# Performance work log

Hardware: AMD Instinct MI355X
Metric: run time of the kernel (lower is better)

Reference implementation:

```python
import jax, jax.numpy as jnp
import numpy as np

C, H, R, INTER = 1024, 16, 16, 2816  # hidden, heads, lora rank, mlp intermediate
B, N = 2, 2048
EPS = 1e-5


def setup_inputs() -> dict:
    key = jax.random.key(0)
    ks = iter(jax.random.split(key, 48))
    w = lambda shape: jax.random.normal(next(ks), shape, jnp.float32) * 0.02
    d = {}
    d["x"] = jax.random.normal(next(ks), (B, N, C), jnp.float32)
    d["y"] = jax.random.normal(next(ks), (B, N, C), jnp.float32)
    d["c"] = jax.random.normal(next(ks), (B, C), jnp.float32)
    # LayerNorms
    d["gx_w"] = jnp.ones((C,)); d["gx_b"] = jnp.zeros((C,))
    d["gy_w"] = jnp.ones((C,)); d["gy_b"] = jnp.zeros((C,))
    # adaLN: SiLU -> Linear(C, 6C)
    d["ada_w"] = w((C, 6 * C)); d["ada_b"] = jnp.zeros((6 * C,))
    # two DoRA cross-attentions
    for p in ("xy", "yx"):
        d[p + "_qkv"] = w((C, 3 * C))
        d[p + "_mag"] = jnp.ones((1, H, 1, 1))
        d[p + "_la"] = w((C, R))
        d[p + "_lb"] = w((R, C))
        d[p + "_proj"] = w((C, C))
    # two HGRN recurrent attentions
    for p in ("ax", "ay"):
        d[p + "_wi"] = w((C, C))
        d[p + "_wf"] = w((C, C))
        d[p + "_wg"] = w((C, C))
        d[p + "_wo"] = w((C, C))
        d[p + "_gn"] = jnp.ones((C,))
    # two gated MLPs
    for p in ("mx", "my"):
        d[p + "_gate"] = w((C, 2 * INTER))
        d[p + "_down"] = w((INTER, C))
    return d


def _ln(v, wgt, b):
    m = v.mean(-1, keepdims=True)
    var = ((v - m) ** 2).mean(-1, keepdims=True)
    return (v - m) / jnp.sqrt(var + EPS) * wgt + b


def _modulate(v, shift, scale):
    return v * (1.0 + scale[:, None, :]) + shift[:, None, :]


def _dora_attn(q_in, Wqkv, mag, la, lb, Wp):
    # NOTE: source ignores key/value args -> self-attention on query stream
    Bq, Nq, Cq = q_in.shape
    D = Cq // H
    qkv = (q_in @ Wqkv).reshape(Bq, Nq, 3, H, D).transpose(2, 0, 3, 1, 4)
    q, k, v = qkv[0], qkv[1], qkv[2]  # [B,H,N,D]
    delta = (q_in @ la) @ lb  # LoRA delta injected into Q
    q = q + mag * delta.reshape(Bq, Nq, H, D).transpose(0, 2, 1, 3)
    attn = jax.nn.softmax(jnp.einsum('bhnd,bhmd->bhnm', q, k) * (D ** -0.5), axis=-1)
    o = jnp.einsum('bhnm,bhmd->bhnd', attn, v).transpose(0, 2, 1, 3).reshape(Bq, Nq, Cq)
    return o @ Wp


def _hgrn_attn(v, wi, wf, wg, wo, gn):
    Bv, Nv, Cv = v.shape
    D = Cv // H
    f = jax.nn.sigmoid(v @ wf)
    i = jax.nn.silu(v @ wi) * (1.0 - f)
    def step(h, ft_it):
        ft, it = ft_it
        h = ft * h + it
        return h, h
    _, hs = jax.lax.scan(step, jnp.zeros((Bv, Cv), v.dtype),
                         (f.transpose(1, 0, 2), i.transpose(1, 0, 2)))
    h = hs.transpose(1, 0, 2).reshape(Bv, Nv, H, D)
    h = h / jnp.sqrt((h * h).mean(-1, keepdims=True) + EPS)  # per-head RMSNorm
    h = (h * gn.reshape(H, D)).reshape(Bv, Nv, Cv)
    return (h * jax.nn.silu(v @ wg)) @ wo


def _mlp(v, wgate, wdown):
    u = v @ wgate
    gate, val = jnp.split(u, 2, axis=-1)
    return (jax.nn.silu(gate) * val) @ wdown


def reference(x, y, c, gx_w, gx_b, gy_w, gy_b, ada_w, ada_b,
              xy_qkv, xy_mag, xy_la, xy_lb, xy_proj,
              yx_qkv, yx_mag, yx_la, yx_lb, yx_proj,
              ax_wi, ax_wf, ax_wg, ax_wo, ax_gn,
              ay_wi, ay_wf, ay_wg, ay_wo, ay_gn,
              mx_gate, mx_down, my_gate, my_down):
    mods = jax.nn.silu(c) @ ada_w + ada_b
    sh_msa, sc_msa, g_msa, sh_mlp, sc_mlp, g_mlp = jnp.split(mods, 6, axis=1)
    x_norm = _ln(x, gx_w, gx_b)
    y_norm = _ln(y, gy_w, gy_b)
    x = x + g_msa[:, None, :] * _dora_attn(x_norm, xy_qkv, xy_mag, xy_la, xy_lb, xy_proj)
    y = y + g_msa[:, None, :] * _dora_attn(y_norm, yx_qkv, yx_mag, yx_la, yx_lb, yx_proj)
    x = x + g_msa[:, None, :] * _hgrn_attn(_modulate(x_norm, sh_msa, sc_msa), ax_wi, ax_wf, ax_wg, ax_wo, ax_gn)
    y = y + g_msa[:, None, :] * _hgrn_attn(_modulate(y_norm, sh_msa, sc_msa), ay_wi, ay_wf, ay_wg, ay_wo, ay_gn)
    x = x + g_mlp[:, None, :] * _mlp(_modulate(_ln(x, gx_w, gx_b), sh_mlp, sc_mlp), mx_gate, mx_down)
    y = y + g_mlp[:, None, :] * _mlp(_modulate(_ln(y, gy_w, gy_b), sh_mlp, sc_mlp), my_gate, my_down)
    return (x, y)
```

## Files before the change

kernel.cpp:

```cpp
#include <hip/hip_runtime.h>
#include <stdint.h>

#define NTOK 2048
#define CDIM 1024
#define ROWS 4096
#define MODS_STRIDE 6144
#define INTERDIM 2816
#define NCHUNK 32
#define CHLEN (NTOK/NCHUNK)

typedef unsigned short u16;
typedef __bf16 bf16x8 __attribute__((ext_vector_type(8)));
typedef float f32x4 __attribute__((ext_vector_type(4)));
typedef u16 u16x8 __attribute__((ext_vector_type(8)));

__device__ __forceinline__ float b2f(u16 u){
  union { unsigned int i; float f; } v; v.i = ((unsigned int)u) << 16; return v.f;
}
__device__ __forceinline__ u16 f2b(float f){
  union { float f; unsigned int i; } v; v.f = f;
  unsigned int i = v.i;
  unsigned int r = i + 0x7FFFu + ((i >> 16) & 1u);
  return (u16)(r >> 16);
}
__device__ __forceinline__ float sigm(float x){ return 1.f/(1.f+__expf(-x)); }
__device__ __forceinline__ float wredsum(float v){
#pragma unroll
  for (int o=32;o>0;o>>=1) v += __shfl_xor(v,o);
  return v;
}
__device__ __forceinline__ void async16(const void* g, void* l){
  __builtin_amdgcn_global_load_lds(
      (const __attribute__((address_space(1))) unsigned int*)g,
      (__attribute__((address_space(3))) unsigned int*)l, 16, 0, 0);
}

__global__ __launch_bounds__(256) void gemm_bt(
    const u16* __restrict__ Ain, const u16* __restrict__ Bt,
    int M, int N, int K, int epi,
    u16* __restrict__ outB,
    float* __restrict__ dest, const float* __restrict__ gate)
{
  __shared__ u16 lA[128*32];
  __shared__ u16 lB[128*32];
  const int m0 = blockIdx.y*128, n0 = blockIdx.x*128;
  const int kchunk = K / gridDim.z;
  const int kbase  = blockIdx.z * kchunk;
  const int tid  = threadIdx.x;
  const int w    = tid>>6, lane = tid&63;
  const int quad = lane>>4, l16 = lane&15;
  const int wr = (w>>1)*64, wc = (w&1)*64;
  f32x4 acc[4][4] = {};
  const int ksteps = kchunk >> 5;
  for (int kt=0; kt<ksteps; ++kt){
    const int k0 = kbase + (kt<<5);
#pragma unroll
    for (int j=0;j<2;++j){
      const int c   = (w*2+j)*64 + lane;
      const int row = c>>2, ke = (c&3)*8;
      async16(Ain + (size_t)(m0+row)*K + k0 + ke, (char*)lA + (size_t)(w*2+j)*1024);
      async16(Bt  + (size_t)(n0+row)*K + k0 + ke, (char*)lB + (size_t)(w*2+j)*1024);
    }
    __syncthreads();
    bf16x8 af[4], bq[4];
#pragma unroll
    for (int t=0;t<4;++t){
      af[t] = *reinterpret_cast<const bf16x8*>(&lA[(wr + t*16 + l16)*32 + quad*8]);
      bq[t] = *reinterpret_cast<const bf16x8*>(&lB[(wc + t*16 + l16)*32 + quad*8]);
    }
#pragma unroll
    for (int i=0;i<4;++i)
#pragma unroll
      for (int j=0;j<4;++j)
        acc[i][j] = __builtin_amdgcn_mfma_f32_16x16x32_bf16(af[i], bq[j], acc[i][j], 0,0,0);
    __syncthreads();
  }
#pragma unroll
  for (int i=0;i<4;++i){
#pragma unroll
    for (int j=0;j<4;++j){
      const int col = n0 + wc + j*16 + l16;
#pragma unroll
      for (int r=0;r<4;++r){
        const int row = m0 + wr + i*16 + quad*4 + r;
        const float v = acc[i][j][r];
        const size_t idx = (size_t)row*N + col;
        if (epi==1){ outB[idx] = f2b(v); }
        else {
          const int b = row >> 11;
          atomicAdd(&dest[idx], gate[b*MODS_STRIDE + col] * v);
        }
      }
    }
  }
}

struct TDesc { const float* src; u16* dst; int rows; int cols; int base; int dstride; int doff; };
struct TPack { TDesc d[16]; };

__global__ __launch_bounds__(256) void transpose_all(TPack p, int nmat)
{
  __shared__ float t[32][33];
  const int bid = blockIdx.x;
  int mi = 0;
#pragma unroll 1
  while (mi+1 < nmat && bid >= p.d[mi+1].base) ++mi;
  const TDesc D = p.d[mi];
  const int tid2   = bid - D.base;
  const int tilesx = D.cols >> 5;
  const int r0 = (tid2 / tilesx) * 32;
  const int c0 = (tid2 % tilesx) * 32;
  const int tx = threadIdx.x & 31, ty = threadIdx.x >> 5;
  for (int i=ty;i<32;i+=8)
    t[i][tx] = D.src[(size_t)(r0+i)*D.cols + c0 + tx];
  __syncthreads();
  for (int i=ty;i<32;i+=8)
    D.dst[(size_t)(c0+i)*D.dstride + D.doff + r0 + tx] = f2b(t[tx][i]);
}

__global__ __launch_bounds__(256) void ln_kernel(
    const float* __restrict__ xin,
    const float* __restrict__ w, const float* __restrict__ bias,
    const float* __restrict__ mods, int sh_off, int sc_off,
    u16* __restrict__ out_norm, u16* __restrict__ out_mod,
    float* __restrict__ out_xw)
{
  const int row = blockIdx.x;
  const int b = row >> 11;
  const int t = threadIdx.x;
  float v[4];
#pragma unroll
  for (int e=0;e<4;++e)
    v[e] = xin[(size_t)row*CDIM + t*4+e];
  float s  = v[0]+v[1]+v[2]+v[3];
  float ss = v[0]*v[0]+v[1]*v[1]+v[2]*v[2]+v[3]*v[3];
  s = wredsum(s); ss = wredsum(ss);
  __shared__ float rs[4], rss[4];
  const int wv = t>>6;
  if ((t&63)==0){ rs[wv]=s; rss[wv]=ss; }
  __syncthreads();
  s  = rs[0]+rs[1]+rs[2]+rs[3];
  ss = rss[0]+rss[1]+rss[2]+rss[3];
  const float mean = s * (1.f/1024.f);
  const float var  = ss * (1.f/1024.f) - mean*mean;
  const float rinv = rsqrtf(var + 1e-5f);
#pragma unroll
  for (int e=0;e<4;++e){
    const int c = t*4+e;
    const float nv = (v[e]-mean)*rinv*w[c] + bias[c];
    if (out_norm) out_norm[(size_t)row*CDIM+c] = f2b(nv);
    if (out_mod){
      const float sc = mods[b*MODS_STRIDE + sc_off + c];
      const float sh = mods[b*MODS_STRIDE + sh_off + c];
      out_mod[(size_t)row*CDIM+c] = f2b(nv*(1.f+sc)+sh);
    }
    if (out_xw) out_xw[(size_t)row*CDIM+c] = v[e];
  }
}

__global__ __launch_bounds__(256) void ada_init(
    const float* __restrict__ ab, float* __restrict__ mods)
{
  const int j = blockIdx.x*256 + threadIdx.x;
  const int jj = (j >= MODS_STRIDE) ? j - MODS_STRIDE : j;
  mods[j] = ab[jj];
}

__global__ __launch_bounds__(256) void ada_split(
    const float* __restrict__ cin, const float* __restrict__ aw,
    float* __restrict__ mods)
{
  const int j  = blockIdx.x*256 + threadIdx.x;
  const int k0 = blockIdx.y*64;
  float s0 = 0.f, s1 = 0.f;
  for (int k=k0; k<k0+64; ++k){
    const float wv = aw[(size_t)k*MODS_STRIDE + j];
    const float c0 = cin[k], c1 = cin[CDIM + k];
    s0 = fmaf(c0*sigm(c0), wv, s0);
    s1 = fmaf(c1*sigm(c1), wv, s1);
  }
  atomicAdd(&mods[j], s0);
  atomicAdd(&mods[MODS_STRIDE + j], s1);
}

__global__ __launch_bounds__(256) void lora_a(
    const u16* __restrict__ xn, const float* __restrict__ la, float* __restrict__ tmp)
{
  const int r = blockIdx.x;
  const int t = threadIdx.x;
  const int n = t & 15, slice = t >> 4;
  float s = 0.f;
  for (int kk=0;kk<64;++kk){
    const int k = slice*64 + kk;
    s = fmaf(b2f(xn[(size_t)r*CDIM + k]), la[k*16 + n], s);
  }
  __shared__ float red[256];
  red[t] = s;
  __syncthreads();
  if (t < 16){
    float tot = 0.f;
#pragma unroll
    for (int sl=0;sl<16;++sl) tot += red[sl*16 + t];
    tmp[r*16 + t] = tot;
  }
}

__global__ __launch_bounds__(256) void lora_b(
    const float* __restrict__ tmp, const float* __restrict__ lb, u16* __restrict__ delta)
{
  const unsigned int idx = blockIdx.x*256u + threadIdx.x;
  const unsigned int r = idx >> 10, c = idx & 1023u;
  float s = 0.f;
#pragma unroll
  for (int j=0;j<16;++j)
    s = fmaf(tmp[r*16 + j], lb[j*CDIM + c], s);
  delta[idx] = f2b(s);
}

__global__ __launch_bounds__(256) void attn_mfma(
    const u16* __restrict__ qkv, const u16* __restrict__ delta,
    const float* __restrict__ mag, u16* __restrict__ AH)
{
  __shared__ u16 Kl[64*72];
  __shared__ u16 Vt[64*72];
  __shared__ u16 Pl[4][16*72];
  const int t = threadIdx.x;
  const int w = t>>6, lane = t&63;
  const int l16 = lane&15, quad = lane>>4;
  const int qt = blockIdx.x, h = blockIdx.y, b = blockIdx.z;
  const size_t rowbase = (size_t)b*NTOK;
  const float magh = mag[h];

  bf16x8 qf[2];
  {
    const size_t gr = rowbase + qt*64 + w*16 + l16;
    const u16* qp = qkv   + gr*3072 + h*64;
    const u16* dp = delta + gr*1024 + h*64;
#pragma unroll
    for (int kw=0; kw<2; ++kw){
      const int d0 = kw*32 + quad*8;
      const u16x8 qa = *reinterpret_cast<const u16x8*>(qp + d0);
      const u16x8 da = *reinterpret_cast<const u16x8*>(dp + d0);
#pragma unroll
      for (int j=0;j<8;++j)
        qf[kw][j] = (__bf16)((b2f(qa[j]) + magh*b2f(da[j])) * 0.125f);
    }
  }

  float l_part = 0.f;
  f32x4 oacc[4] = {};

  for (int kb=0; kb<32; ++kb){
    __syncthreads();
#pragma unroll
    for (int it=0; it<2; ++it){
      const int e = it*256 + t;
      const int key = e>>3, dc = (e&7)*8;
      const u16x8 kv = *reinterpret_cast<const u16x8*>(
          qkv + (rowbase + kb*64 + key)*3072 + 1024 + h*64 + dc);
      *reinterpret_cast<u16x8*>(&Kl[key*72 + dc]) = kv;
    }
#pragma unroll
    for (int it=0; it<2; ++it){
      const int d0 = (w*2 + it)*8;
      const u16x8 vv = *reinterpret_cast<const u16x8*>(
          qkv + (rowbase + kb*64 + lane)*3072 + 2048 + h*64 + d0);
#pragma unroll
      for (int j=0;j<8;++j)
        Vt[(d0+j)*72 + lane] = vv[j];
    }
    __syncthreads();

    f32x4 sacc[4] = {};
#pragma unroll
    for (int kw=0; kw<2; ++kw){
#pragma unroll
      for (int mt=0; mt<4; ++mt){
        const bf16x8 af = *reinterpret_cast<const bf16x8*>(
            &Kl[(mt*16 + l16)*72 + kw*32 + quad*8]);
        sacc[mt] = __builtin_amdgcn_mfma_f32_16x16x32_bf16(af, qf[kw], sacc[mt], 0,0,0);
      }
    }

#pragma unroll
    for (int mt=0;mt<4;++mt)
#pragma unroll
      for (int r=0;r<4;++r){
        const float pv = __expf(sacc[mt][r]);
        sacc[mt][r] = pv;
        l_part += pv;
      }

#pragma unroll
    for (int mt=0;mt<4;++mt)
#pragma unroll
      for (int rp=0; rp<2; ++rp){
        const unsigned hi = __float_as_uint(sacc[mt][rp*2+1]);
        const unsigned lo = __float_as_uint(sacc[mt][rp*2]);
        *reinterpret_cast<unsigned*>(&Pl[w][l16*72 + mt*16 + quad*4 + rp*2]) =
            (hi & 0xFFFF0000u) | (lo >> 16);
      }

#pragma unroll
    for (int kw=0; kw<2; ++kw){
      const bf16x8 pa = *reinterpret_cast<const bf16x8*>(
          &Pl[w][l16*72 + kw*32 + quad*8]);
#pragma unroll
      for (int dt=0; dt<4; ++dt){
        const bf16x8 vb = *reinterpret_cast<const bf16x8*>(
            &Vt[(dt*16 + l16)*72 + kw*32 + quad*8]);
        oacc[dt] = __builtin_amdgcn_mfma_f32_16x16x32_bf16(pa, vb, oacc[dt], 0,0,0);
      }
    }
  }

  float l_run = l_part;
  l_run += __shfl_xor(l_run, 16);
  l_run += __shfl_xor(l_run, 32);

  float li4[4];
#pragma unroll
  for (int r=0;r<4;++r) li4[r] = __shfl(l_run, quad*4+r);
#pragma unroll
  for (int r=0;r<4;++r){
    const size_t grow = rowbase + qt*64 + w*16 + quad*4 + r;
#pragma unroll
    for (int dt=0; dt<4; ++dt)
      AH[grow*2048 + h*64 + dt*16 + l16] = f2b(oacc[dt][r] / li4[r]);
  }
}

__global__ __launch_bounds__(256) void scan_p1(
    const u16* __restrict__ FIG, float* __restrict__ cA, float* __restrict__ cH)
{
  const unsigned int idx = blockIdx.x*256u + threadIdx.x;
  const unsigned int c = idx & 1023u, chunk = (idx>>10)&(NCHUNK-1), b = idx>>15;
  float A = 1.f, h = 0.f;
  const size_t base = ((size_t)b*NTOK + chunk*CHLEN) * 3072;
  for (int t=0;t<CHLEN;++t){
    const float F = b2f(FIG[base + (size_t)t*3072 + c]);
    const float I = b2f(FIG[base + (size_t)t*3072 + 1024 + c]);
    const float f = sigm(F);
    const float il = I*sigm(I) * (1.f - f);
    A *= f;
    h = fmaf(f, h, il);
  }
  cA[idx] = A; cH[idx] = h;
}

__global__ __launch_bounds__(256) void scan_p2(
    const float* __restrict__ cA, const float* __restrict__ cH, float* __restrict__ Hinit)
{
  const unsigned int idx = blockIdx.x*256u + threadIdx.x;
  const unsigned int b = idx>>10, c = idx&1023u;
  float h = 0.f;
#pragma unroll
  for (int ch=0;ch<NCHUNK;++ch){
    const unsigned int q = (b*NCHUNK + ch)*1024 + c;
    Hinit[q] = h;
    h = fmaf(cA[q], h, cH[q]);
  }
}

__global__ __launch_bounds__(256) void scan_p3(
    const u16* __restrict__ FIG, const float* __restrict__ Hinit, u16* __restrict__ Hb)
{
  const unsigned int idx = blockIdx.x*256u + threadIdx.x;
  const unsigned int c = idx & 1023u, chunk = (idx>>10)&(NCHUNK-1), b = idx>>15;
  float h = Hinit[idx];
  const size_t base = ((size_t)b*NTOK + chunk*CHLEN) * 3072;
  const size_t obase = ((size_t)b*NTOK + chunk*CHLEN) * CDIM;
  for (int t=0;t<CHLEN;++t){
    const float F = b2f(FIG[base + (size_t)t*3072 + c]);
    const float I = b2f(FIG[base + (size_t)t*3072 + 1024 + c]);
    const float f = sigm(F);
    const float il = I*sigm(I) * (1.f - f);
    h = fmaf(f, h, il);
    Hb[obase + (size_t)t*CDIM + c] = f2b(h);
  }
}

__global__ __launch_bounds__(256) void hgrn_post(
    const u16* __restrict__ Hb, const u16* __restrict__ FIG,
    const float* __restrict__ gn, u16* __restrict__ AH)
{
  const int row = blockIdx.x;
  const int t = threadIdx.x;
  float hv[4]; float ss = 0.f;
#pragma unroll
  for (int e=0;e<4;++e){
    hv[e] = b2f(Hb[(size_t)row*CDIM + t*4 + e]);
    ss = fmaf(hv[e], hv[e], ss);
  }
#pragma unroll
  for (int o=1;o<16;o<<=1) ss += __shfl_xor(ss, o);
  const float rinv = rsqrtf(ss*(1.f/64.f) + 1e-5f);
#pragma unroll
  for (int e=0;e<4;++e){
    const int c = t*4+e;
    const float g = b2f(FIG[(size_t)row*3072 + 2048 + c]);
    AH[(size_t)row*2048 + 1024 + c] = f2b(hv[e]*rinv*gn[c] * g*sigm(g));
  }
}

__global__ __launch_bounds__(256) void act_kernel(
    const u16* __restrict__ U, u16* __restrict__ A)
{
  const unsigned int i = blockIdx.x*256u + threadIdx.x;
  const unsigned int r = i / INTERDIM, j = i % INTERDIM;
  const float g = b2f(U[(size_t)r*(2*INTERDIM) + j]);
  const float v = b2f(U[(size_t)r*(2*INTERDIM) + INTERDIM + j]);
  A[i] = f2b(g*sigm(g)*v);
}

__global__ __launch_bounds__(256) void store_out(
    const float* __restrict__ xw, float* __restrict__ out)
{
  const unsigned int i = blockIdx.x*256u + threadIdx.x;
  out[i] = xw[i];
}

__global__ __launch_bounds__(256) void fill_fail(float* __restrict__ out)
{
  const unsigned int i = blockIdx.x*256u + threadIdx.x;
  out[i] = 1234.5f;
}

static void run_stream(hipStream_t stream,
    const float* Xin, const float* LNW, const float* LNB,
    const float* MAG, const float* LA, const float* LBw, const float* GN,
    float* mods, float* xw, float* outp,
    const u16* WqkvT, const u16* WpwT, const u16* WhgrnT,
    const u16* WgateT, const u16* WdownT,
    u16* x_norm, u16* v_h, u16* qkvb, float* tmp, u16* delta, u16* AH,
    float* cA, float* cH, float* Hinit, u16* U, u16* actb)
{
  u16* FIG    = qkvb;
  u16* Hb     = delta;
  u16* mlp_in = x_norm;

  ln_kernel<<<ROWS,256,0,stream>>>(Xin, LNW, LNB, mods, 0, 1024, x_norm, v_h, xw);

  gemm_bt<<<dim3(24,32),256,0,stream>>>(x_norm, WqkvT, ROWS,3072,1024, 1, qkvb, nullptr, nullptr);
  lora_a<<<ROWS,256,0,stream>>>(x_norm, LA, tmp);
  lora_b<<<ROWS*CDIM/256,256,0,stream>>>(tmp, LBw, delta);
  attn_mfma<<<dim3(32,16,2),256,0,stream>>>(qkvb, delta, MAG, AH);

  gemm_bt<<<dim3(24,32),256,0,stream>>>(v_h, WhgrnT, ROWS,3072,1024, 1, FIG, nullptr, nullptr);
  scan_p1<<<2*NCHUNK*1024/256,256,0,stream>>>(FIG, cA, cH);
  scan_p2<<<8,256,0,stream>>>(cA, cH, Hinit);
  scan_p3<<<2*NCHUNK*1024/256,256,0,stream>>>(FIG, Hinit, Hb);
  hgrn_post<<<ROWS,256,0,stream>>>(Hb, FIG, GN, AH);

  gemm_bt<<<dim3(8,32,2),256,0,stream>>>(AH, WpwT, ROWS,1024,2048, 2, nullptr, xw, mods+2048);

  ln_kernel<<<ROWS,256,0,stream>>>(xw, LNW, LNB, mods, 3072, 4096, nullptr, mlp_in, nullptr);
  gemm_bt<<<dim3(44,32),256,0,stream>>>(mlp_in, WgateT, ROWS,5632,1024, 1, U, nullptr, nullptr);
  act_kernel<<<ROWS*INTERDIM/256,256,0,stream>>>(U, actb);
  gemm_bt<<<dim3(8,32,4),256,0,stream>>>(actb, WdownT, ROWS,1024,2816, 2, nullptr, xw, mods+5120);

  store_out<<<ROWS*CDIM/256,256,0,stream>>>(xw, outp);
}

extern "C" void kernel_launch(void* const* d_in, const int* in_sizes, int n_in,
                              void* d_out, int out_size, void* d_ws, size_t ws_size,
                              hipStream_t stream)
{
  const float* X    = (const float*)d_in[0];
  const float* Y    = (const float*)d_in[1];
  const float* Cc   = (const float*)d_in[2];
  const float* GXW  = (const float*)d_in[3];
  const float* GXB  = (const float*)d_in[4];
  const float* GYW  = (const float*)d_in[5];
  const float* GYB  = (const float*)d_in[6];
  const float* ADAW = (const float*)d_in[7];
  const float* ADAB = (const float*)d_in[8];
  const float* XY_QKV = (const float*)d_in[9];
  const float* XY_MAG = (const float*)d_in[10];
  const float* XY_LA  = (const float*)d_in[11];
  const float* XY_LB  = (const float*)d_in[12];
  const float* XY_PROJ= (const float*)d_in[13];
  const float* YX_QKV = (const float*)d_in[14];
  const float* YX_MAG = (const float*)d_in[15];
  const float* YX_LA  = (const float*)d_in[16];
  const float* YX_LB  = (const float*)d_in[17];
  const float* YX_PROJ= (const float*)d_in[18];
  const float* AX_WI = (const float*)d_in[19];
  const float* AX_WF = (const float*)d_in[20];
  const float* AX_WG = (const float*)d_in[21];
  const float* AX_WO = (const float*)d_in[22];
  const float* AX_GN = (const float*)d_in[23];
  const float* AY_WI = (const float*)d_in[24];
  const float* AY_WF = (const float*)d_in[25];
  const float* AY_WG = (const float*)d_in[26];
  const float* AY_WO = (const float*)d_in[27];
  const float* AY_GN = (const float*)d_in[28];
  const float* MX_GATE = (const float*)d_in[29];
  const float* MX_DOWN = (const float*)d_in[30];
  const float* MY_GATE = (const float*)d_in[31];
  const float* MY_DOWN = (const float*)d_in[32];
  float* OUT = (float*)d_out;

  char* p = (char*)d_ws;
  size_t off = 0;
  auto alloc = [&](size_t bytes)->char*{
    char* r = p + off;
    off = (off + bytes + 255) & ~(size_t)255;
    return r;
  };
  float* mods  = (float*)alloc(2*MODS_STRIDE*sizeof(float));
  float* xw_x  = (float*)alloc((size_t)ROWS*CDIM*sizeof(float));
  float* xw_y  = (float*)alloc((size_t)ROWS*CDIM*sizeof(float));
  u16* WqkvT0  = (u16*)alloc((size_t)3072*1024*2);
  u16* WqkvT1  = (u16*)alloc((size_t)3072*1024*2);
  u16* WpwT0   = (u16*)alloc((size_t)1024*2048*2);
  u16* WpwT1   = (u16*)alloc((size_t)1024*2048*2);
  u16* WhgrnT0 = (u16*)alloc((size_t)3072*1024*2);
  u16* WhgrnT1 = (u16*)alloc((size_t)3072*1024*2);
  u16* WgateT0 = (u16*)alloc((size_t)5632*1024*2);
  u16* WgateT1 = (u16*)alloc((size_t)5632*1024*2);
  u16* WdownT0 = (u16*)alloc((size_t)1024*2816*2);
  u16* WdownT1 = (u16*)alloc((size_t)1024*2816*2);
  u16* x_norm  = (u16*)alloc((size_t)ROWS*CDIM*2);
  u16* v_h     = (u16*)alloc((size_t)ROWS*CDIM*2);
  u16* qkvb    = (u16*)alloc((size_t)ROWS*3072*2);
  float* tmp   = (float*)alloc((size_t)ROWS*16*sizeof(float));
  u16* delta   = (u16*)alloc((size_t)ROWS*CDIM*2);
  u16* AH      = (u16*)alloc((size_t)ROWS*2048*2);
  float* cA    = (float*)alloc((size_t)2*NCHUNK*1024*sizeof(float));
  float* cH    = (float*)alloc((size_t)2*NCHUNK*1024*sizeof(float));
  float* Hinit = (float*)alloc((size_t)2*NCHUNK*1024*sizeof(float));
  u16* U       = (u16*)alloc((size_t)ROWS*5632*2);
  u16* actb    = (u16*)alloc((size_t)ROWS*INTERDIM*2);

  if (off > ws_size){
    fill_fail<<<(2*ROWS*CDIM)/256,256,0,stream>>>(OUT);
    return;
  }

  ada_init<<<2*MODS_STRIDE/256,256,0,stream>>>(ADAB, mods);
  ada_split<<<dim3(MODS_STRIDE/256,16),256,0,stream>>>(Cc, ADAW, mods);

  TPack tp; int base = 0; int ndesc = 0;
  auto add = [&](const float* s, u16* d2, int rows, int cols, int dstride, int doff){
    tp.d[ndesc].src = s; tp.d[ndesc].dst = d2;
    tp.d[ndesc].rows = rows; tp.d[ndesc].cols = cols; tp.d[ndesc].base = base;
    tp.d[ndesc].dstride = dstride; tp.d[ndesc].doff = doff;
    base += (rows>>5)*(cols>>5); ++ndesc;
  };
  add(XY_QKV,  WqkvT0, 1024, 3072, 1024, 0);
  add(XY_PROJ, WpwT0,  1024, 1024, 2048, 0);
  add(AX_WO,   WpwT0,  1024, 1024, 2048, 1024);
  add(AX_WF, WhgrnT0,               1024, 1024, 1024, 0);
  add(AX_WI, WhgrnT0 + 1024*1024,   1024, 1024, 1024, 0);
  add(AX_WG, WhgrnT0 + 2*1024*1024, 1024, 1024, 1024, 0);
  add(MX_GATE, WgateT0, 1024, 5632, 1024, 0);
  add(MX_DOWN, WdownT0, 2816, 1024, 2816, 0);
  add(YX_QKV,  WqkvT1, 1024, 3072, 1024, 0);
  add(YX_PROJ, WpwT1,  1024, 1024, 2048, 0);
  add(AY_WO,   WpwT1,  1024, 1024, 2048, 1024);
  add(AY_WF, WhgrnT1,               1024, 1024, 1024, 0);
  add(AY_WI, WhgrnT1 + 1024*1024,   1024, 1024, 1024, 0);
  add(AY_WG, WhgrnT1 + 2*1024*1024, 1024, 1024, 1024, 0);
  add(MY_GATE, WgateT1, 1024, 5632, 1024, 0);
  add(MY_DOWN, WdownT1, 2816, 1024, 2816, 0);
  transpose_all<<<base,256,0,stream>>>(tp, ndesc);

  run_stream(stream, X, GXW, GXB, XY_MAG, XY_LA, XY_LB, AX_GN,
             mods, xw_x, OUT,
             WqkvT0, WpwT0, WhgrnT0, WgateT0, WdownT0,
             x_norm, v_h, qkvb, tmp, delta, AH,
             cA, cH, Hinit, U, actb);

  run_stream(stream, Y, GYW, GYB, YX_MAG, YX_LA, YX_LB, AY_GN,
             mods, xw_y, OUT + (size_t)ROWS*CDIM,
             WqkvT1, WpwT1, WhgrnT1, WgateT1, WdownT1,
             x_norm, v_h, qkvb, tmp, delta, AH,
             cA, cH, Hinit, U, actb);
}
```

Baseline: 1.374 ms.

## Triple-buffer GEMM LDS tiles with async prefetch and XCD-aware block swizzle

```diff
diff --git a/kernel.cpp b/kernel.cpp
--- a/kernel.cpp
+++ b/kernel.cpp
@@ -41,40 +41,67 @@
     u16* __restrict__ outB,
     float* __restrict__ dest, const float* __restrict__ gate)
 {
-  __shared__ u16 lA[128*32];
-  __shared__ u16 lB[128*32];
-  const int m0 = blockIdx.y*128, n0 = blockIdx.x*128;
+  __shared__ u16 lA[3][128*32];
+  __shared__ u16 lB[3][128*32];
+
+  const int nwg  = gridDim.x * gridDim.y;
+  const int orig = blockIdx.y * gridDim.x + blockIdx.x;
+  const int qch  = nwg >> 3, rch = nwg & 7;
+  const int xcd  = orig & 7, loc = orig >> 3;
+  const int swz  = (xcd < rch ? xcd*(qch+1) : rch*(qch+1) + (xcd-rch)*qch) + loc;
+  const int m0 = (swz / gridDim.x) * 128;
+  const int n0 = (swz % gridDim.x) * 128;
+
   const int kchunk = K / gridDim.z;
   const int kbase  = blockIdx.z * kchunk;
   const int tid  = threadIdx.x;
   const int w    = tid>>6, lane = tid&63;
   const int quad = lane>>4, l16 = lane&15;
   const int wr = (w>>1)*64, wc = (w&1)*64;
-  f32x4 acc[4][4] = {};
   const int ksteps = kchunk >> 5;
-  for (int kt=0; kt<ksteps; ++kt){
+
+  auto stage = [&](int kt, int s){
     const int k0 = kbase + (kt<<5);
 #pragma unroll
     for (int j=0;j<2;++j){
       const int c   = (w*2+j)*64 + lane;
       const int row = c>>2, ke = (c&3)*8;
-      async16(Ain + (size_t)(m0+row)*K + k0 + ke, (char*)lA + (size_t)(w*2+j)*1024);
-      async16(Bt  + (size_t)(n0+row)*K + k0 + ke, (char*)lB + (size_t)(w*2+j)*1024);
-    }
-    __syncthreads();
+      async16(Ain + (size_t)(m0+row)*K + k0 + ke, (char*)(&lA[s][0]) + (size_t)(w*2+j)*1024);
+      async16(Bt  + (size_t)(n0+row)*K + k0 + ke, (char*)(&lB[s][0]) + (size_t)(w*2+j)*1024);
+    }
+  };
+
+  f32x4 acc[4][4] = {};
+  stage(0,0);
+  if (ksteps > 1) stage(1,1);
+
+  int cur = 0;
+  for (int kt=0; kt<ksteps; ++kt){
+    if (kt+1 < ksteps) asm volatile("s_waitcnt vmcnt(4)" ::: "memory");
+    else               asm volatile("s_waitcnt vmcnt(0)" ::: "memory");
+    __builtin_amdgcn_s_barrier();
+    __builtin_amdgcn_sched_barrier(0);
+
+    if (kt+2 < ksteps){
+      int sb = cur + 2; if (sb >= 3) sb -= 3;
+      stage(kt+2, sb);
+    }
+
     bf16x8 af[4], bq[4];
 #pragma unroll
     for (int t=0;t<4;++t){
-      af[t] = *reinterpret_cast<const bf16x8*>(&lA[(wr + t*16 + l16)*32 + quad*8]);
-      bq[t] = *reinterpret_cast<const bf16x8*>(&lB[(wc + t*16 + l16)*32 + quad*8]);
+      af[t] = *reinterpret_cast<const bf16x8*>(&lA[cur][(wr + t*16 + l16)*32 + quad*8]);
+      bq[t] = *reinterpret_cast<const bf16x8*>(&lB[cur][(wc + t*16 + l16)*32 + quad*8]);
     }
 #pragma unroll
     for (int i=0;i<4;++i)
 #pragma unroll
       for (int j=0;j<4;++j)
         acc[i][j] = __builtin_amdgcn_mfma_f32_16x16x32_bf16(af[i], bq[j], acc[i][j], 0,0,0);
-    __syncthreads();
-  }
+
+    ++cur; if (cur >= 3) cur = 0;
+  }
+
 #pragma unroll
   for (int i=0;i<4;++i){
 #pragma unroll
```

Measured after the change: 1.332 ms. 1.03x faster.

## Rewrite bf16 GEMM with 256x256 tiles, double-buffered swizzled LDS pipeline

Applied to the files above, without the earlier changes.

```diff
diff --git a/kernel.cpp b/kernel.cpp
--- a/kernel.cpp
+++ b/kernel.cpp
@@ -35,59 +35,184 @@
       (__attribute__((address_space(3))) unsigned int*)l, 16, 0, 0);
 }
 
-__global__ __launch_bounds__(256) void gemm_bt(
+__global__ __launch_bounds__(512) void gemm_bt(
     const u16* __restrict__ Ain, const u16* __restrict__ Bt,
     int M, int N, int K, int epi,
     u16* __restrict__ outB,
     float* __restrict__ dest, const float* __restrict__ gate)
 {
-  __shared__ u16 lA[128*32];
-  __shared__ u16 lB[128*32];
-  const int m0 = blockIdx.y*128, n0 = blockIdx.x*128;
+  __shared__ u16 smem[2][2][2][8192];
+
+  const int nwg  = gridDim.x * gridDim.y;
+  const int orig = blockIdx.y * gridDim.x + blockIdx.x;
+  const int qch  = nwg >> 3, rch = nwg & 7;
+  const int xcd  = orig & 7, loc = orig >> 3;
+  const int swzb = (xcd < rch ? xcd*(qch+1) : rch*(qch+1) + (xcd-rch)*qch) + loc;
+  const int m0 = (swzb / gridDim.x) * 256;
+  const int n0 = (swzb % gridDim.x) * 256;
+
   const int kchunk = K / gridDim.z;
   const int kbase  = blockIdx.z * kchunk;
-  const int tid  = threadIdx.x;
-  const int w    = tid>>6, lane = tid&63;
-  const int quad = lane>>4, l16 = lane&15;
-  const int wr = (w>>1)*64, wc = (w&1)*64;
-  f32x4 acc[4][4] = {};
-  const int ksteps = kchunk >> 5;
-  for (int kt=0; kt<ksteps; ++kt){
-    const int k0 = kbase + (kt<<5);
-#pragma unroll
-    for (int j=0;j<2;++j){
-      const int c   = (w*2+j)*64 + lane;
-      const int row = c>>2, ke = (c&3)*8;
-      async16(Ain + (size_t)(m0+row)*K + k0 + ke, (char*)lA + (size_t)(w*2+j)*1024);
-      async16(Bt  + (size_t)(n0+row)*K + k0 + ke, (char*)lB + (size_t)(w*2+j)*1024);
-    }
-    __syncthreads();
-    bf16x8 af[4], bq[4];
-#pragma unroll
-    for (int t=0;t<4;++t){
-      af[t] = *reinterpret_cast<const bf16x8*>(&lA[(wr + t*16 + l16)*32 + quad*8]);
-      bq[t] = *reinterpret_cast<const bf16x8*>(&lB[(wc + t*16 + l16)*32 + quad*8]);
-    }
-#pragma unroll
-    for (int i=0;i<4;++i)
-#pragma unroll
-      for (int j=0;j<4;++j)
-        acc[i][j] = __builtin_amdgcn_mfma_f32_16x16x32_bf16(af[i], bq[j], acc[i][j], 0,0,0);
-    __syncthreads();
-  }
-#pragma unroll
-  for (int i=0;i<4;++i){
+  const int NT = kchunk >> 6;
+
+  const int tid = threadIdx.x;
+  const int w = tid >> 6, lane = tid & 63;
+  const int quad = lane >> 4, l16 = lane & 15;
+  const int wm = w >> 2, wn = w & 3;
+  const int sx = (l16 & 7) << 4;
+
+  int soff[2];
+#pragma unroll
+  for (int j=0;j<2;++j){
+    const int row = (w*2 + j)*8 + (lane >> 3);
+    soff[j] = row*(K*2) + (((lane & 7) ^ (row & 7)) << 4);
+  }
+
+  const char* pA0 = (const char*)(Ain + (size_t)m0*K       + kbase);
+  const char* pA1 = (const char*)(Ain + (size_t)(m0+128)*K + kbase);
+  const char* pB0 = (const char*)(Bt  + (size_t)n0*K       + kbase);
+  const char* pB1 = (const char*)(Bt  + (size_t)(n0+128)*K + kbase);
+
+  auto stage = [&](const char* base, int t, u16* region){
+#pragma unroll
+    for (int j=0;j<2;++j)
+      async16(base + (size_t)t*128 + soff[j], (char*)region + (w*2+j)*1024);
+  };
+
+  f32x4 acc[8][4] = {};
+  bf16x8 af[4][2];
+  bf16x8 bq[4][2];
+
+  stage(pA0, 0, &smem[0][0][0][0]);
+  stage(pA1, 0, &smem[0][0][1][0]);
+  stage(pB0, 0, &smem[0][1][0][0]);
+  stage(pB1, 0, &smem[0][1][1][0]);
+  if (NT > 1){
+    stage(pA0, 1, &smem[1][0][0][0]);
+    asm volatile("s_waitcnt vmcnt(2)" ::: "memory");
+  } else {
+    asm volatile("s_waitcnt vmcnt(0)" ::: "memory");
+  }
+  __builtin_amdgcn_s_barrier();
+
+#pragma unroll 1
+  for (int t=0; t<NT; ++t){
+    const int s  = t & 1;
+    const int s1 = s ^ 1;
+    const char* Ah = (const char*)&smem[s][0][wm][0];
+    const char* Bh = (const char*)&smem[s][1][wn>>1][0];
+    const int bb = (wn & 1) * 64;
+
+#pragma unroll
+    for (int mf=0; mf<4; ++mf)
+#pragma unroll
+      for (int ks=0; ks<2; ++ks){
+        const int b = ((mf*16 + l16)*128 + ks*64 + quad*16) ^ sx;
+        af[mf][ks] = *reinterpret_cast<const bf16x8*>(Ah + b);
+      }
+#pragma unroll
+    for (int nf=0; nf<2; ++nf)
+#pragma unroll
+      for (int ks=0; ks<2; ++ks){
+        const int b = ((bb + nf*16 + l16)*128 + ks*64 + quad*16) ^ sx;
+        bq[nf][ks] = *reinterpret_cast<const bf16x8*>(Bh + b);
+      }
+    if (t+1 < NT) stage(pA1, t+1, &smem[s1][0][1][0]);
+    __builtin_amdgcn_sched_barrier(0);
+    __builtin_amdgcn_s_barrier();
+    asm volatile("s_waitcnt lgkmcnt(0)" ::: "memory");
+    __builtin_amdgcn_sched_barrier(0);
+    __builtin_amdgcn_s_setprio(1);
+#pragma unroll
+    for (int mf=0; mf<4; ++mf)
+#pragma unroll
+      for (int nf=0; nf<2; ++nf)
+#pragma unroll
+        for (int ks=0; ks<2; ++ks)
+          acc[mf][nf] = __builtin_amdgcn_mfma_f32_16x16x32_bf16(af[mf][ks], bq[nf][ks], acc[mf][nf], 0,0,0);
+    __builtin_amdgcn_s_setprio(0);
+    __builtin_amdgcn_sched_barrier(0);
+    __builtin_amdgcn_s_barrier();
+
+#pragma unroll
+    for (int nf=0; nf<2; ++nf)
+#pragma unroll
+      for (int ks=0; ks<2; ++ks){
+        const int b = ((bb + (2+nf)*16 + l16)*128 + ks*64 + quad*16) ^ sx;
+        bq[2+nf][ks] = *reinterpret_cast<const bf16x8*>(Bh + b);
+      }
+    if (t+1 < NT) stage(pB0, t+1, &smem[s1][1][0][0]);
+    __builtin_amdgcn_sched_barrier(0);
+    __builtin_amdgcn_s_barrier();
+    asm volatile("s_waitcnt lgkmcnt(0)" ::: "memory");
+    __builtin_amdgcn_sched_barrier(0);
+    __builtin_amdgcn_s_setprio(1);
+#pragma unroll
+    for (int mf=0; mf<4; ++mf)
+#pragma unroll
+      for (int nf=0; nf<2; ++nf)
+#pragma unroll
+        for (int ks=0; ks<2; ++ks)
+          acc[mf][2+nf] = __builtin_amdgcn_mfma_f32_16x16x32_bf16(af[mf][ks], bq[2+nf][ks], acc[mf][2+nf], 0,0,0);
+    __builtin_amdgcn_s_setprio(0);
+    __builtin_amdgcn_sched_barrier(0);
+    __builtin_amdgcn_s_barrier();
+
+#pragma unroll
+    for (int mf=0; mf<4; ++mf)
+#pragma unroll
+      for (int ks=0; ks<2; ++ks){
+        const int b = ((64 + mf*16 + l16)*128 + ks*64 + quad*16) ^ sx;
+        af[mf][ks] = *reinterpret_cast<const bf16x8*>(Ah + b);
+      }
+    if (t+1 < NT) stage(pB1, t+1, &smem[s1][1][1][0]);
+    __builtin_amdgcn_sched_barrier(0);
+    __builtin_amdgcn_s_barrier();
+    asm volatile("s_waitcnt lgkmcnt(0)" ::: "memory");
+    __builtin_amdgcn_sched_barrier(0);
+    __builtin_amdgcn_s_setprio(1);
+#pragma unroll
+    for (int mf=0; mf<4; ++mf)
+#pragma unroll
+      for (int nf=0; nf<2; ++nf)
+#pragma unroll
+        for (int ks=0; ks<2; ++ks)
+          acc[4+mf][2+nf] = __builtin_amdgcn_mfma_f32_16x16x32_bf16(af[mf][ks], bq[2+nf][ks], acc[4+mf][2+nf], 0,0,0);
+    __builtin_amdgcn_s_setprio(0);
+    __builtin_amdgcn_sched_barrier(0);
+    __builtin_amdgcn_s_barrier();
+
+    if (t+2 < NT) stage(pA0, t+2, &smem[s][0][0][0]);
+    __builtin_amdgcn_sched_barrier(0);
+    __builtin_amdgcn_s_barrier();
+    __builtin_amdgcn_s_setprio(1);
+#pragma unroll
+    for (int mf=0; mf<4; ++mf)
+#pragma unroll
+      for (int nf=0; nf<2; ++nf)
+#pragma unroll
+        for (int ks=0; ks<2; ++ks)
+          acc[4+mf][nf] = __builtin_amdgcn_mfma_f32_16x16x32_bf16(af[mf][ks], bq[nf][ks], acc[4+mf][nf], 0,0,0);
+    __builtin_amdgcn_s_setprio(0);
+    __builtin_amdgcn_sched_barrier(0);
+    if (t+2 < NT) asm volatile("s_waitcnt vmcnt(2)" ::: "memory");
+    else          asm volatile("s_waitcnt vmcnt(0)" ::: "memory");
+    __builtin_amdgcn_s_barrier();
+  }
+
+#pragma unroll
+  for (int i=0;i<8;++i){
+    const int row = m0 + wm*128 + (i>>2)*64 + (i&3)*16 + quad*4;
 #pragma unroll
     for (int j=0;j<4;++j){
-      const int col = n0 + wc + j*16 + l16;
+      const int col = n0 + wn*64 + j*16 + l16;
 #pragma unroll
       for (int r=0;r<4;++r){
-        const int row = m0 + wr + i*16 + quad*4 + r;
         const float v = acc[i][j][r];
-        const size_t idx = (size_t)row*N + col;
+        const size_t idx = (size_t)(row + r)*N + col;
         if (epi==1){ outB[idx] = f2b(v); }
         else {
-          const int b = row >> 11;
+          const int b = (row + r) >> 11;
           atomicAdd(&dest[idx], gate[b*MODS_STRIDE + col] * v);
         }
       }
@@ -441,23 +566,23 @@
 
   ln_kernel<<<ROWS,256,0,stream>>>(Xin, LNW, LNB, mods, 0, 1024, x_norm, v_h, xw);
 
-  gemm_bt<<<dim3(24,32),256,0,stream>>>(x_norm, WqkvT, ROWS,3072,1024, 1, qkvb, nullptr, nullptr);
+  gemm_bt<<<dim3(12,16),512,0,stream>>>(x_norm, WqkvT, ROWS,3072,1024, 1, qkvb, nullptr, nullptr);
   lora_a<<<ROWS,256,0,stream>>>(x_norm, LA, tmp);
   lora_b<<<ROWS*CDIM/256,256,0,stream>>>(tmp, LBw, delta);
   attn_mfma<<<dim3(32,16,2),256,0,stream>>>(qkvb, delta, MAG, AH);
 
-  gemm_bt<<<dim3(24,32),256,0,stream>>>(v_h, WhgrnT, ROWS,3072,1024, 1, FIG, nullptr, nullptr);
+  gemm_bt<<<dim3(12,16),512,0,stream>>>(v_h, WhgrnT, ROWS,3072,1024, 1, FIG, nullptr, nullptr);
   scan_p1<<<2*NCHUNK*1024/256,256,0,stream>>>(FIG, cA, cH);
   scan_p2<<<8,256,0,stream>>>(cA, cH, Hinit);
   scan_p3<<<2*NCHUNK*1024/256,256,0,stream>>>(FIG, Hinit, Hb);
   hgrn_post<<<ROWS,256,0,stream>>>(Hb, FIG, GN, AH);
 
-  gemm_bt<<<dim3(8,32,2),256,0,stream>>>(AH, WpwT, ROWS,1024,2048, 2, nullptr, xw, mods+2048);
+  gemm_bt<<<dim3(4,16,4),512,0,stream>>>(AH, WpwT, ROWS,1024,2048, 2, nullptr, xw, mods+2048);
 
   ln_kernel<<<ROWS,256,0,stream>>>(xw, LNW, LNB, mods, 3072, 4096, nullptr, mlp_in, nullptr);
-  gemm_bt<<<dim3(44,32),256,0,stream>>>(mlp_in, WgateT, ROWS,5632,1024, 1, U, nullptr, nullptr);
+  gemm_bt<<<dim3(22,16),512,0,stream>>>(mlp_in, WgateT, ROWS,5632,1024, 1, U, nullptr, nullptr);
   act_kernel<<<ROWS*INTERDIM/256,256,0,stream>>>(U, actb);
-  gemm_bt<<<dim3(8,32,4),256,0,stream>>>(actb, WdownT, ROWS,1024,2816, 2, nullptr, xw, mods+5120);
+  gemm_bt<<<dim3(4,16,4),512,0,stream>>>(actb, WdownT, ROWS,1024,2816, 2, nullptr, xw, mods+5120);
 
   store_out<<<ROWS*CDIM/256,256,0,stream>>>(xw, outp);
 }
```

Result: faster. 1.324 ms (-3.6%).
